# Kernel tuning notes

Hardware: AMD Instinct MI355X
Metric: run time of the kernel (lower is better)

The kernel has to match this reference:

```python
import jax, jax.numpy as jnp
import numpy as np
import math

D_MODEL = 512
N_HEAD = 8
D_K = D_MODEL // N_HEAD
BN_EPS = 1e-5


def setup_inputs() -> dict:
    key = jax.random.key(0)
    ks = jax.random.split(key, 24)
    B, L = 4, 2048
    s = 0.02
    inp = {
        'query': jax.random.normal(ks[0], (B, L, D_MODEL), jnp.float32),
        'key':   jax.random.normal(ks[1], (B, L, D_MODEL), jnp.float32),
        'value': jax.random.normal(ks[2], (B, L, D_MODEL), jnp.float32),
        # multi-scale conv (kernel sizes 3 and 5)
        'conv_w3': jax.random.normal(ks[3], (D_MODEL, D_MODEL, 3), jnp.float32) * s,
        'conv_b3': jnp.zeros((D_MODEL,), jnp.float32),
        'conv_w5': jax.random.normal(ks[4], (D_MODEL, D_MODEL, 5), jnp.float32) * s,
        'conv_b5': jnp.zeros((D_MODEL,), jnp.float32),
        # batchnorm over 2*d_model channels (inference mode, running stats)
        'bn_gamma': jnp.ones((2 * D_MODEL,), jnp.float32),
        'bn_beta':  jnp.zeros((2 * D_MODEL,), jnp.float32),
        'bn_mean':  jnp.zeros((2 * D_MODEL,), jnp.float32),
        'bn_var':   jnp.ones((2 * D_MODEL,), jnp.float32),
        # linear projections (torch layout: [out, in])
        'wq':  jax.random.normal(ks[5], (D_MODEL, D_MODEL), jnp.float32) * s,
        'bq':  jnp.zeros((D_MODEL,), jnp.float32),
        'wkl': jax.random.normal(ks[6], (D_MODEL, 2 * D_MODEL), jnp.float32) * s,
        'bkl': jnp.zeros((D_MODEL,), jnp.float32),
        'wkg': jax.random.normal(ks[7], (D_MODEL, D_MODEL), jnp.float32) * s,
        'bkg': jnp.zeros((D_MODEL,), jnp.float32),
        'wv':  jax.random.normal(ks[8], (D_MODEL, D_MODEL), jnp.float32) * s,
        'bv':  jnp.zeros((D_MODEL,), jnp.float32),
        'wo':  jax.random.normal(ks[9], (D_MODEL, D_MODEL), jnp.float32) * s,
        'bo':  jnp.zeros((D_MODEL,), jnp.float32),
    }
    return inp


def _conv1d_same(x_ncl, w_oik, b, pad):
    # x: [B, C_in, L], w: [C_out, C_in, K]
    y = jax.lax.conv_general_dilated(
        x_ncl, w_oik, window_strides=(1,), padding=[(pad, pad)],
        dimension_numbers=('NCH', 'OIH', 'NCH'))
    return y + b[None, :, None]


def _heads(x, B, L):
    # [B, L, D] -> [B, L, H, d_k]
    return x.reshape(B, L, N_HEAD, D_K)


def reference(query, key, value, conv_w3, conv_b3, conv_w5, conv_b5,
              bn_gamma, bn_beta, bn_mean, bn_var,
              wq, bq, wkl, bkl, wkg, bkg, wv, bv, wo, bo):
    B, L, _ = query.shape
    # local key path: multi-scale conv over sequence dim
    k_ncl = key.transpose(0, 2, 1)                      # [B, D, L]
    c3 = _conv1d_same(k_ncl, conv_w3, conv_b3, 1)       # [B, D, L]
    c5 = _conv1d_same(k_ncl, conv_w5, conv_b5, 2)       # [B, D, L]
    cat = jnp.concatenate([c3, c5], axis=1)             # [B, 2D, L]
    bn = (cat - bn_mean[None, :, None]) * (bn_gamma[None, :, None]
          * jax.lax.rsqrt(bn_var[None, :, None] + BN_EPS)) + bn_beta[None, :, None]
    key_local = bn.transpose(0, 2, 1)                   # [B, L, 2D]

    q  = _heads(query @ wq.T + bq, B, L)                # [B, L, H, dk]
    kl = _heads(key_local @ wkl.T + bkl, B, L)
    kg = _heads(key @ wkg.T + bkg, B, L)
    v  = _heads(value @ wv.T + bv, B, L)

    scale = 1.0 / math.sqrt(D_K)
    s_loc = jnp.einsum('bqhd,bkhd->bhqk', q, kl) * scale
    s_glo = jnp.einsum('bqhd,bkhd->bhqk', q, kg) * scale
    a_loc = jax.nn.softmax(s_loc, axis=-1)
    a_glo = jax.nn.softmax(s_glo, axis=-1)
    x = jnp.einsum('bhqk,bkhd->bqhd', a_loc, v) + jnp.einsum('bhqk,bkhd->bqhd', a_glo, v)
    x = x.reshape(B, L, N_HEAD * D_K)
    return x @ wo.T + bo
```

## Files before the change

### kernel.cpp

```cpp
#include <hip/hip_runtime.h>
#include <hip/hip_bf16.h>

#define D_MODEL 512
#define SEQ_L   2048
#define NBATCH  4
#define BLROWS  8192
#define BN_EPS_F 1e-5f
#define QK_SCALE 0.18033688011112042f

typedef __attribute__((ext_vector_type(8))) short bf16x8;
typedef __attribute__((ext_vector_type(4))) float f32x4;
typedef __attribute__((ext_vector_type(16))) float f32x16;
typedef __attribute__((ext_vector_type(2))) int i32x2;

__device__ __forceinline__ unsigned short f2bf(float f){
  union { float f; unsigned u; } x; x.f = f;
  return (unsigned short)((x.u + 0x7fffu + ((x.u >> 16) & 1u)) >> 16);
}
__device__ __forceinline__ unsigned pack2bf(float a, float b){
  return (unsigned)f2bf(a) | ((unsigned)f2bf(b) << 16);
}
__device__ __forceinline__ unsigned cvt_pk(float a, float b){
  unsigned r;
  asm("v_cvt_pk_bf16_f32 %0, %1, %2" : "=v"(r) : "v"(a), "v"(b));
  return r;
}
__device__ __forceinline__ float exp2fast(float x){
  float r;
  asm("v_exp_f32 %0, %1" : "=v"(r) : "v"(x));
  return r;
}
__device__ __forceinline__ float max3f(float a, float b, float c){
  float r;
  asm("v_max3_f32 %0, %1, %2, %3" : "=v"(r) : "v"(a), "v"(b), "v"(c));
  return r;
}
__device__ __forceinline__ f32x4 mfma16(bf16x8 a, bf16x8 b, f32x4 c){
  return __builtin_amdgcn_mfma_f32_16x16x32_bf16(a, b, c, 0, 0, 0);
}
__device__ __forceinline__ f32x16 mfma32(bf16x8 a, bf16x8 b, f32x16 c){
  return __builtin_amdgcn_mfma_f32_32x32x16_bf16(a, b, c, 0, 0, 0);
}
__device__ __forceinline__ bf16x8 ldb8(const unsigned short* p){
  return *reinterpret_cast<const bf16x8*>(p);
}
__device__ __forceinline__ void gld16(const void* g, void* l){
  __builtin_amdgcn_global_load_lds(
      (const __attribute__((address_space(1))) unsigned*)g,
      (__attribute__((address_space(3))) unsigned*)l, 16, 0, 0);
}

__global__ void k_cast3(const float* __restrict__ s0, const float* __restrict__ s1,
                        const float* __restrict__ s2, unsigned short* __restrict__ d0,
                        unsigned short* __restrict__ d1, unsigned short* __restrict__ d2,
                        int n){
  const int z = blockIdx.y;
  const float* s = (z == 0) ? s0 : (z == 1) ? s1 : s2;
  unsigned short* d = (z == 0) ? d0 : (z == 1) ? d1 : d2;
  int i = (blockIdx.x * blockDim.x + threadIdx.x) * 4;
  if (i >= n) return;
  float4 v = *reinterpret_cast<const float4*>(s + i);
  uint2 o;
  o.x = pack2bf(v.x, v.y);
  o.y = pack2bf(v.z, v.w);
  *reinterpret_cast<uint2*>(d + i) = o;
}

__global__ void k_cast4(const float* __restrict__ s0, const float* __restrict__ s1,
                        const float* __restrict__ s2, const float* __restrict__ s3,
                        unsigned short* __restrict__ d0, unsigned short* __restrict__ d1,
                        unsigned short* __restrict__ d2, unsigned short* __restrict__ d3,
                        int n, float sc0){
  const int z = blockIdx.y;
  const float* s = (z == 0) ? s0 : (z == 1) ? s1 : (z == 2) ? s2 : s3;
  unsigned short* d = (z == 0) ? d0 : (z == 1) ? d1 : (z == 2) ? d2 : d3;
  const float sc = (z == 0) ? sc0 : 1.f;
  int i = (blockIdx.x * blockDim.x + threadIdx.x) * 4;
  if (i >= n) return;
  float4 v = *reinterpret_cast<const float4*>(s + i);
  uint2 o;
  o.x = pack2bf(v.x * sc, v.y * sc);
  o.y = pack2bf(v.z * sc, v.w * sc);
  *reinterpret_cast<uint2*>(d + i) = o;
}

__global__ void k_acat(const float* __restrict__ wkl, const float* __restrict__ gamma,
                       const float* __restrict__ var, unsigned short* __restrict__ Acat){
  int idx = blockIdx.x * blockDim.x + threadIdx.x;
  int o = idx >> 10, ch = idx & 1023;
  int c = (ch < 512) ? (512 + ch) : (ch - 512);
  float a = gamma[c] * rsqrtf(var[c] + BN_EPS_F);
  Acat[idx] = f2bf(wkl[o * 1024 + c] * a);
}

__global__ void k_bcat(const float* __restrict__ w3, const float* __restrict__ w5,
                       unsigned short* __restrict__ Bcat){
  int idx = blockIdx.x * blockDim.x + threadIdx.x;
  int t = idx >> 19; int r = idx & 524287;
  int ci = r >> 10, ch = r & 1023;
  float v;
  if (ch < 512) v = w5[ch * 2560 + ci * 5 + t];
  else {
    int c3 = ch - 512;
    v = (t >= 1 && t <= 3) ? w3[c3 * 1536 + ci * 3 + (t - 1)] : 0.0f;
  }
  Bcat[idx] = f2bf(v);
}

__global__ void k_beff(const float* __restrict__ wkl, const float* __restrict__ gamma,
                       const float* __restrict__ beta, const float* __restrict__ mean,
                       const float* __restrict__ var, const float* __restrict__ cb3,
                       const float* __restrict__ cb5, const float* __restrict__ bkl,
                       float* __restrict__ beff){
  const int o = blockIdx.x * 4 + (threadIdx.x >> 6);
  const int lane = threadIdx.x & 63;
  float acc = 0.f;
  for (int c = lane; c < 1024; c += 64){
    float a = gamma[c] * rsqrtf(var[c] + BN_EPS_F);
    float cb = (c < 512) ? cb3[c] : cb5[c - 512];
    acc += wkl[o * 1024 + c] * (a * cb + beta[c] - a * mean[c]);
  }
#pragma unroll
  for (int off = 32; off; off >>= 1) acc += __shfl_down(acc, off);
  if (lane == 0) beff[o] = acc + bkl[o];
}

template<int MODE, int BN = 128>
__global__ __launch_bounds__(256, 2) void k_gemm(
    const unsigned short* __restrict__ A, const unsigned short* __restrict__ Bm,
    void* __restrict__ Cp, const float* __restrict__ bias,
    const float* __restrict__ bias1, const float* __restrict__ bias2, float bias_scale,
    int M, int N, int K, int lda, int ldb, int ldc,
    long sAz, long sBz, long sCz, const unsigned short* __restrict__ zeros)
{
  __shared__ unsigned short As[128 * 64];
  __shared__ unsigned short Bs[BN * 64];
  constexpr int NW2 = BN / 32;
  const int m0 = blockIdx.x * 128, n0 = blockIdx.y * BN;
  const unsigned short* Az = A + (long)blockIdx.z * sAz;
  const unsigned short* Bz = Bm + (long)blockIdx.z * sBz;
  const float* bz = bias; float bs = bias_scale;
  if (MODE == 3){
    if (blockIdx.z == 1){ bz = bias1; bs = 1.f; }
    else if (blockIdx.z == 2){ bz = bias2; bs = 1.f; }
  }
  const int tid = threadIdx.x, wid = tid >> 6, lane = tid & 63;
  const int l15 = lane & 15, hq = lane >> 4;
  const int wr = wid >> 1, wc = wid & 1;
  f32x4 acc[4][NW2];
#pragma unroll
  for (int m = 0; m < 4; ++m)
#pragma unroll
    for (int n = 0; n < NW2; ++n) acc[m][n] = f32x4{0.f, 0.f, 0.f, 0.f};
  const int nkt = K >> 6;
  const int wv4 = wid * 512;
  const int srow = tid >> 3;
  const int scol = (tid & 7) * 8;
  for (int kt = 0; kt < nkt; ++kt){
    __syncthreads();
    if (MODE == 2){
      const int t = kt >> 3; const int ci0 = (kt & 7) << 6;
#pragma unroll
      for (int i = 0; i < 4; ++i){
        int row = srow + i * 32;
        int gr = m0 + row;
        int sl = (gr & (SEQ_L - 1)) + t - 2;
        const unsigned short* sp = ((unsigned)sl < (unsigned)SEQ_L)
            ? (Az + (long)(gr + t - 2) * lda + ci0 + scol) : (zeros + scol);
        gld16(sp, As + i * 2048 + wv4);
      }
#pragma unroll
      for (int i = 0; i < BN / 32; ++i){
        int row = srow + i * 32;
        gld16(Bz + (long)t * 262144 + (long)(n0 + row) * ldb + ci0 + scol,
              Bs + i * 2048 + wv4);
      }
    } else {
      const int k0 = kt << 6;
#pragma unroll
      for (int i = 0; i < 4; ++i){
        int row = srow + i * 32;
        gld16(Az + (long)(m0 + row) * lda + k0 + scol, As + i * 2048 + wv4);
      }
#pragma unroll
      for (int i = 0; i < BN / 32; ++i){
        int row = srow + i * 32;
        gld16(Bz + (long)(n0 + row) * ldb + k0 + scol, Bs + i * 2048 + wv4);
      }
    }
    __syncthreads();
#pragma unroll
    for (int ks = 0; ks < 2; ++ks){
      const int kb = ks * 32 + 8 * hq;
      bf16x8 af[4], bfr[NW2];
#pragma unroll
      for (int m = 0; m < 4; ++m) af[m] = ldb8(As + (wr * 64 + m * 16 + l15) * 64 + kb);
#pragma unroll
      for (int n = 0; n < NW2; ++n)
        bfr[n] = ldb8(Bs + (wc * (BN / 2) + n * 16 + l15) * 64 + kb);
#pragma unroll
      for (int m = 0; m < 4; ++m)
#pragma unroll
        for (int n = 0; n < NW2; ++n) acc[m][n] = mfma16(af[m], bfr[n], acc[m][n]);
    }
  }
  const int crow0 = m0 + wr * 64, ccol0 = n0 + wc * (BN / 2);
#pragma unroll
  for (int n = 0; n < NW2; ++n){
    int col = ccol0 + n * 16 + l15;
    float bv = bz ? bz[col] * bs : 0.f;
#pragma unroll
    for (int m = 0; m < 4; ++m){
      int rowb = crow0 + m * 16 + 4 * hq;
#pragma unroll
      for (int r = 0; r < 4; ++r){
        float v = acc[m][n][r] + bv;
        long off = (long)(rowb + r) * ldc + col + (long)blockIdx.z * sCz;
        if (MODE == 1) ((float*)Cp)[off] = v;
        else ((unsigned short*)Cp)[off] = f2bf(v);
      }
    }
  }
}

__global__ __launch_bounds__(256) void k_transpose(const unsigned short* __restrict__ V,
                                                   unsigned short* __restrict__ Vt){
  __shared__ unsigned short t_lds[64][72];
  const int l0 = blockIdx.x * 64, d0 = blockIdx.y * 64, b = blockIdx.z;
  const int tid = threadIdx.x;
  const int rr = tid >> 3, cc = (tid & 7) * 8;
#pragma unroll
  for (int p = 0; p < 2; ++p){
    int r = rr + p * 32;
    bf16x8 v = ldb8(V + ((long)(b * SEQ_L + l0 + r)) * D_MODEL + d0 + cc);
#pragma unroll
    for (int j = 0; j < 8; ++j) t_lds[r][cc + j] = (unsigned short)v[j];
  }
  __syncthreads();
#pragma unroll
  for (int p = 0; p < 2; ++p){
    int dr = rr + p * 32;
    bf16x8 o;
#pragma unroll
    for (int j = 0; j < 8; ++j) o[j] = (short)t_lds[cc + j][dr];
    *reinterpret_cast<bf16x8*>(Vt + ((long)(b * D_MODEL + d0 + dr)) * SEQ_L + l0 + cc) = o;
  }
}

__global__ __launch_bounds__(256, 2) void k_attn(
    const unsigned short* __restrict__ Q, const unsigned short* __restrict__ KLp,
    const unsigned short* __restrict__ KGp, const unsigned short* __restrict__ Vt,
    unsigned short* __restrict__ X)
{
  __shared__ unsigned short KLb[2][64 * 64];
  __shared__ unsigned short KGb[2][64 * 64];
  __shared__ unsigned short Vb [2][64 * 64];

  const int lin = blockIdx.x + (blockIdx.y << 4);
  const int sw  = ((lin & 7) << 6) + (lin >> 3);
  const int qi = sw & 15, bh = sw >> 4;
  const int b = bh >> 3, hb = (bh & 7) << 6;
  const int tid = threadIdx.x, wid = tid >> 6, lane = tid & 63;
  const int l31 = lane & 31, hi = lane >> 5;
  const int s7 = l31 & 7;
  const int q0 = qi * 128 + wid * 32;
  const long rb = (long)b * SEQ_L;

  const long qrow = (rb + q0 + l31) * D_MODEL + hb + hi * 8;
  bf16x8 qf[4];
#pragma unroll
  for (int ch = 0; ch < 4; ++ch) qf[ch] = ldb8(Q + qrow + ch * 16);

  f32x16 o_l[2], o_g[2];
#pragma unroll
  for (int dt = 0; dt < 2; ++dt){ o_l[dt] = 0.f; o_g[dt] = 0.f; }
  float m_l = -1e30f, s_l = 0.f, m_g = -1e30f, s_g = 0.f;

  auto stage = [&](const unsigned short* gbase, long rowstride, unsigned short* lb){
#pragma unroll
    for (int i = 0; i < 2; ++i){
      const int idx0 = (i * 4 + wid) * 64;
      const int idx = idx0 + lane;
      const int row = idx >> 3, cl = idx & 7;
      const int cg = cl ^ (row & 7);
      gld16(gbase + (long)row * rowstride + cg * 8, lb + idx0 * 8);
    }
  };

  auto qk = [&](const unsigned short* Kb_, f32x16& sa, f32x16& sb){
    __builtin_amdgcn_s_setprio(1);
#pragma unroll
    for (int ch = 0; ch < 4; ++ch){
      bf16x8 k0 = ldb8(Kb_ + l31 * 64 + (((hi + 2 * ch) ^ s7) * 8));
      bf16x8 k1 = ldb8(Kb_ + (l31 + 32) * 64 + (((hi + 2 * ch) ^ s7) * 8));
      sa = mfma32(k0, qf[ch], sa);
      sb = mfma32(k1, qf[ch], sb);
    }
    __builtin_amdgcn_s_setprio(0);
  };

  auto softmax_pv = [&](f32x16& sa, f32x16& sb, float& mrun, float& srun,
                        f32x16 (&o)[2], bf16x8 (&vf)[2][4]){
    float u[8];
#pragma unroll
    for (int r = 0; r < 8; ++r)
      u[r] = max3f(sa[r], sa[r + 8], fmaxf(sb[r], sb[r + 8]));
    float pm = max3f(max3f(u[0], u[1], u[2]), max3f(u[3], u[4], u[5]),
                     fmaxf(u[6], u[7]));
    i32x2 pr = __builtin_amdgcn_permlane32_swap(__float_as_int(pm), __float_as_int(pm), false, false);
    pm = max3f(pm, __int_as_float(pr[0]), __int_as_float(pr[1]));
    if (__any(pm > mrun + 11.0f)){
      float mn = fmaxf(mrun, pm);
      float rs = exp2fast(mrun - mn);
      srun *= rs; mrun = mn;
#pragma unroll
      for (int r = 0; r < 16; ++r){ o[0][r] *= rs; o[1][r] *= rs; }
    }
#pragma unroll
    for (int r = 0; r < 16; ++r) sa[r] = exp2fast(sa[r] - mrun);
#pragma unroll
    for (int r = 0; r < 16; ++r) sb[r] = exp2fast(sb[r] - mrun);
    float w[8];
#pragma unroll
    for (int r = 0; r < 8; ++r) w[r] = (sa[r] + sa[r + 8]) + (sb[r] + sb[r + 8]);
    float sum = ((w[0] + w[1]) + (w[2] + w[3])) + ((w[4] + w[5]) + (w[6] + w[7]));
    i32x2 sr = __builtin_amdgcn_permlane32_swap(__float_as_int(sum), __float_as_int(sum), false, false);
    srun += __int_as_float(sr[0]) + __int_as_float(sr[1]);
    unsigned uu[2][4][2];
#pragma unroll
    for (int r4 = 0; r4 < 4; ++r4){
      uu[0][r4][0] = cvt_pk(sa[r4 * 4 + 0], sa[r4 * 4 + 1]);
      uu[0][r4][1] = cvt_pk(sa[r4 * 4 + 2], sa[r4 * 4 + 3]);
      uu[1][r4][0] = cvt_pk(sb[r4 * 4 + 0], sb[r4 * 4 + 1]);
      uu[1][r4][1] = cvt_pk(sb[r4 * 4 + 2], sb[r4 * 4 + 3]);
    }
    __builtin_amdgcn_s_setprio(1);
#pragma unroll
    for (int kc = 0; kc < 4; ++kc){
      const int t = kc >> 1, kk = kc & 1;
      i32x2 rA = __builtin_amdgcn_permlane32_swap((int)uu[t][2 * kk][0], (int)uu[t][2 * kk + 1][0], false, false);
      i32x2 rB = __builtin_amdgcn_permlane32_swap((int)uu[t][2 * kk][1], (int)uu[t][2 * kk + 1][1], false, false);
      union { bf16x8 v; int w_[4]; } pb;
      pb.w_[0] = rA[0]; pb.w_[1] = rB[0]; pb.w_[2] = rA[1]; pb.w_[3] = rB[1];
      o[0] = mfma32(vf[0][kc], pb.v, o[0]);
      o[1] = mfma32(vf[1][kc], pb.v, o[1]);
    }
    __builtin_amdgcn_s_setprio(0);
  };

  const unsigned short* klg = KLp + rb * D_MODEL + hb;
  const unsigned short* kgg = KGp + rb * D_MODEL + hb;
  const unsigned short* vtg = Vt + ((long)b * D_MODEL + hb) * SEQ_L;

  stage(klg, D_MODEL, KLb[0]);
  stage(kgg, D_MODEL, KGb[0]);
  stage(vtg, SEQ_L,  Vb[0]);
  asm volatile("s_waitcnt vmcnt(0)" ::: "memory");
  __syncthreads();

  int cur = 0;
#pragma unroll 1
  for (int t = 0; t < SEQ_L / 64; ++t){
    const int nxt = cur ^ 1;
    if (t < SEQ_L / 64 - 1){
      const long kvn = (long)(t + 1) * 64;
      stage(klg + kvn * D_MODEL, D_MODEL, KLb[nxt]);
      stage(kgg + kvn * D_MODEL, D_MODEL, KGb[nxt]);
      stage(vtg + kvn,           SEQ_L,   Vb[nxt]);
    }
    bf16x8 vf[2][4];
#pragma unroll
    for (int dt = 0; dt < 2; ++dt)
#pragma unroll
      for (int kc = 0; kc < 4; ++kc)
        vf[dt][kc] = ldb8(Vb[cur] + (l31 + dt * 32) * 64 + (((kc * 2 + hi) ^ s7) * 8));
    f32x16 sa = 0.f, sb = 0.f;
    qk(KLb[cur], sa, sb);
    softmax_pv(sa, sb, m_l, s_l, o_l, vf);
    f32x16 ga = 0.f, gb = 0.f;
    qk(KGb[cur], ga, gb);
    softmax_pv(ga, gb, m_g, s_g, o_g, vf);
    asm volatile("s_waitcnt vmcnt(0)" ::: "memory");
    __syncthreads();
    cur = nxt;
  }

  const float il = 1.f / s_l, ig = 1.f / s_g;
  const long xrow = (rb + q0 + l31) * D_MODEL + hb + hi * 4;
#pragma unroll
  for (int dt = 0; dt < 2; ++dt)
#pragma unroll
    for (int r4 = 0; r4 < 4; ++r4){
      float v0 = o_l[dt][r4 * 4 + 0] * il + o_g[dt][r4 * 4 + 0] * ig;
      float v1 = o_l[dt][r4 * 4 + 1] * il + o_g[dt][r4 * 4 + 1] * ig;
      float v2 = o_l[dt][r4 * 4 + 2] * il + o_g[dt][r4 * 4 + 2] * ig;
      float v3 = o_l[dt][r4 * 4 + 3] * il + o_g[dt][r4 * 4 + 3] * ig;
      uint2 pk2; pk2.x = cvt_pk(v0, v1); pk2.y = cvt_pk(v2, v3);
      *reinterpret_cast<uint2*>(X + xrow + dt * 32 + r4 * 8) = pk2;
    }
}

extern "C" void kernel_launch(void* const* d_in, const int* in_sizes, int n_in,
                              void* d_out, int out_size, void* d_ws, size_t ws_size,
                              hipStream_t stream)
{
  const float* query = (const float*)d_in[0];
  const float* key   = (const float*)d_in[1];
  const float* value = (const float*)d_in[2];
  const float* w3    = (const float*)d_in[3];
  const float* cb3   = (const float*)d_in[4];
  const float* w5    = (const float*)d_in[5];
  const float* cb5   = (const float*)d_in[6];
  const float* gamma = (const float*)d_in[7];
  const float* beta  = (const float*)d_in[8];
  const float* mean  = (const float*)d_in[9];
  const float* var   = (const float*)d_in[10];
  const float* wq    = (const float*)d_in[11];
  const float* bq    = (const float*)d_in[12];
  const float* wkl   = (const float*)d_in[13];
  const float* bkl   = (const float*)d_in[14];
  const float* wkg   = (const float*)d_in[15];
  const float* bkg   = (const float*)d_in[16];
  const float* wv    = (const float*)d_in[17];
  const float* bv    = (const float*)d_in[18];
  const float* wo    = (const float*)d_in[19];
  const float* bo    = (const float*)d_in[20];

  char* ws = (char*)d_ws;
  const size_t MB = 1024 * 1024;
  unsigned short* qb   = (unsigned short*)(ws + 0 * MB);
  unsigned short* kb   = (unsigned short*)(ws + 8 * MB);
  unsigned short* vb   = (unsigned short*)(ws + 16 * MB);
  unsigned short* Qm   = (unsigned short*)(ws + 24 * MB);
  unsigned short* KGm  = (unsigned short*)(ws + 32 * MB);
  unsigned short* Vm   = (unsigned short*)(ws + 40 * MB);
  unsigned short* KLm  = (unsigned short*)(ws + 48 * MB);
  unsigned short* Vt   = qb;
  unsigned short* Xm   = vb;
  unsigned short* Bcat = Qm;
  unsigned short* Acat = KGm;
  unsigned short* Weff = (unsigned short*)(ws + 56 * MB);
  unsigned short* wqb  = (unsigned short*)(ws + 56 * MB + 2621440);
  unsigned short* wkgb = wqb + 262144;
  unsigned short* wvb  = wqb + 524288;
  unsigned short* wob  = wqb + 786432;
  float*          beff = (float*)(ws + 61 * MB);
  unsigned short* zeros= (unsigned short*)(ws + 61 * MB + 4096);

  hipMemsetAsync(zeros, 0, 256, stream);

  const int NQKV = BLROWS * D_MODEL;
  const int NW   = D_MODEL * D_MODEL;
  dim3 tb(256);
  k_cast3<<<dim3(NQKV / 1024, 3), tb, 0, stream>>>(query, key, value, qb, kb, vb, NQKV);
  k_cast4<<<dim3(NW / 1024, 4), tb, 0, stream>>>(wq, wkg, wv, wo, wqb, wkgb, wvb, wob,
                                                 NW, QK_SCALE);
  k_acat<<<(512 * 1024) / 256, tb, 0, stream>>>(wkl, gamma, var, Acat);
  k_bcat<<<(5 * 512 * 1024) / 256, tb, 0, stream>>>(w3, w5, Bcat);
  k_beff<<<128, tb, 0, stream>>>(wkl, gamma, beta, mean, var, cb3, cb5, bkl, beff);

  k_gemm<0><<<dim3(4, 4, 5), tb, 0, stream>>>(Acat, Bcat, Weff,
      nullptr, nullptr, nullptr, 0.f,
      512, 512, 1024, 1024, 1024, 512, 0L, 524288L, 262144L, nullptr);

  k_gemm<3><<<dim3(64, 4, 3), tb, 0, stream>>>(qb, wqb, Qm,
      bq, bkg, bv, QK_SCALE,
      BLROWS, D_MODEL, D_MODEL, D_MODEL, D_MODEL, D_MODEL,
      4194304L, 262144L, 4194304L, nullptr);

  k_gemm<2, 64><<<dim3(64, 8), tb, 0, stream>>>(kb, Weff, KLm,
      beff, nullptr, nullptr, 1.f,
      BLROWS, D_MODEL, 2560, D_MODEL, D_MODEL, D_MODEL, 0L, 0L, 0L, zeros);

  k_transpose<<<dim3(32, 8, 4), tb, 0, stream>>>(Vm, Vt);
  k_attn<<<dim3(16, 32), tb, 0, stream>>>(Qm, KLm, KGm, Vt, Xm);

  k_gemm<1><<<dim3(64, 4), tb, 0, stream>>>(Xm, wob, d_out,
      bo, nullptr, nullptr, 1.f,
      BLROWS, D_MODEL, D_MODEL, D_MODEL, D_MODEL, D_MODEL, 0L, 0L, 0L, nullptr);
}
```

Measured before the change: 245.8 us.

## Split local and global attention paths across separate wave groups in attention kernel

The attention block grows from 256 to 512 threads. Waves 0-3 now handle the local-key softmax path and waves 4-7 handle the global-key path, where before each wave ran both paths one after the other. Staging work is spread over all eight waves, and V fragments are read from LDS inside the PV loop instead of being preloaded. At the end, the global path writes its normalized output to shared memory and the local-path waves add it in and store. This doubles the number of waves working on the same tile and lowers per-wave register pressure, at the cost of an extra LDS reduction and barrier and fewer resident blocks per CU.

```diff
diff --git a/kernel.cpp b/kernel.cpp
--- a/kernel.cpp
+++ b/kernel.cpp
@@ -247,23 +247,22 @@
   }
 }
 
-__global__ __launch_bounds__(256, 2) void k_attn(
+__global__ __launch_bounds__(512, 2) void k_attn(
     const unsigned short* __restrict__ Q, const unsigned short* __restrict__ KLp,
     const unsigned short* __restrict__ KGp, const unsigned short* __restrict__ Vt,
     unsigned short* __restrict__ X)
 {
-  __shared__ unsigned short KLb[2][64 * 64];
-  __shared__ unsigned short KGb[2][64 * 64];
-  __shared__ unsigned short Vb [2][64 * 64];
+  __shared__ unsigned short smem[6][4096];
 
   const int lin = blockIdx.x + (blockIdx.y << 4);
   const int sw  = ((lin & 7) << 6) + (lin >> 3);
   const int qi = sw & 15, bh = sw >> 4;
   const int b = bh >> 3, hb = (bh & 7) << 6;
   const int tid = threadIdx.x, wid = tid >> 6, lane = tid & 63;
+  const int path = wid >> 2, wg = wid & 3;
   const int l31 = lane & 31, hi = lane >> 5;
   const int s7 = l31 & 7;
-  const int q0 = qi * 128 + wid * 32;
+  const int q0 = qi * 128 + wg * 32;
   const long rb = (long)b * SEQ_L;
 
   const long qrow = (rb + q0 + l31) * D_MODEL + hb + hi * 8;
@@ -271,23 +270,41 @@
 #pragma unroll
   for (int ch = 0; ch < 4; ++ch) qf[ch] = ldb8(Q + qrow + ch * 16);
 
-  f32x16 o_l[2], o_g[2];
-#pragma unroll
-  for (int dt = 0; dt < 2; ++dt){ o_l[dt] = 0.f; o_g[dt] = 0.f; }
-  float m_l = -1e30f, s_l = 0.f, m_g = -1e30f, s_g = 0.f;
+  f32x16 o[2];
+  o[0] = 0.f; o[1] = 0.f;
+  float mrun = -1e30f, srun = 0.f;
 
   auto stage = [&](const unsigned short* gbase, long rowstride, unsigned short* lb){
-#pragma unroll
-    for (int i = 0; i < 2; ++i){
-      const int idx0 = (i * 4 + wid) * 64;
-      const int idx = idx0 + lane;
-      const int row = idx >> 3, cl = idx & 7;
-      const int cg = cl ^ (row & 7);
-      gld16(gbase + (long)row * rowstride + cg * 8, lb + idx0 * 8);
-    }
+    const int idx0 = wid * 64;
+    const int idx = idx0 + lane;
+    const int row = idx >> 3, cl = idx & 7;
+    const int cg = cl ^ (row & 7);
+    gld16(gbase + (long)row * rowstride + cg * 8, lb + idx0 * 8);
   };
 
-  auto qk = [&](const unsigned short* Kb_, f32x16& sa, f32x16& sb){
+  const unsigned short* klg = KLp + rb * D_MODEL + hb;
+  const unsigned short* kgg = KGp + rb * D_MODEL + hb;
+  const unsigned short* vtg = Vt + ((long)b * D_MODEL + hb) * SEQ_L;
+
+  stage(klg, D_MODEL, smem[0]);
+  stage(kgg, D_MODEL, smem[2]);
+  stage(vtg, SEQ_L,  smem[4]);
+  asm volatile("s_waitcnt vmcnt(0)" ::: "memory");
+  __syncthreads();
+
+  int cur = 0;
+#pragma unroll 1
+  for (int t = 0; t < SEQ_L / 64; ++t){
+    const int nxt = cur ^ 1;
+    if (t < SEQ_L / 64 - 1){
+      const long kvn = (long)(t + 1) * 64;
+      stage(klg + kvn * D_MODEL, D_MODEL, smem[nxt]);
+      stage(kgg + kvn * D_MODEL, D_MODEL, smem[2 + nxt]);
+      stage(vtg + kvn,           SEQ_L,   smem[4 + nxt]);
+    }
+    const unsigned short* Kb_ = path ? smem[2 + cur] : smem[cur];
+    const unsigned short* Vb_ = smem[4 + cur];
+    f32x16 sa = 0.f, sb = 0.f;
     __builtin_amdgcn_s_setprio(1);
 #pragma unroll
     for (int ch = 0; ch < 4; ++ch){
@@ -297,10 +314,6 @@
       sb = mfma32(k1, qf[ch], sb);
     }
     __builtin_amdgcn_s_setprio(0);
-  };
-
-  auto softmax_pv = [&](f32x16& sa, f32x16& sb, float& mrun, float& srun,
-                        f32x16 (&o)[2], bf16x8 (&vf)[2][4]){
     float u[8];
 #pragma unroll
     for (int r = 0; r < 8; ++r)
@@ -337,67 +350,47 @@
     __builtin_amdgcn_s_setprio(1);
 #pragma unroll
     for (int kc = 0; kc < 4; ++kc){
-      const int t = kc >> 1, kk = kc & 1;
-      i32x2 rA = __builtin_amdgcn_permlane32_swap((int)uu[t][2 * kk][0], (int)uu[t][2 * kk + 1][0], false, false);
-      i32x2 rB = __builtin_amdgcn_permlane32_swap((int)uu[t][2 * kk][1], (int)uu[t][2 * kk + 1][1], false, false);
+      const int tt = kc >> 1, kk = kc & 1;
+      i32x2 rA = __builtin_amdgcn_permlane32_swap((int)uu[tt][2 * kk][0], (int)uu[tt][2 * kk + 1][0], false, false);
+      i32x2 rB = __builtin_amdgcn_permlane32_swap((int)uu[tt][2 * kk][1], (int)uu[tt][2 * kk + 1][1], false, false);
       union { bf16x8 v; int w_[4]; } pb;
       pb.w_[0] = rA[0]; pb.w_[1] = rB[0]; pb.w_[2] = rA[1]; pb.w_[3] = rB[1];
-      o[0] = mfma32(vf[0][kc], pb.v, o[0]);
-      o[1] = mfma32(vf[1][kc], pb.v, o[1]);
+      bf16x8 v0 = ldb8(Vb_ + l31 * 64 + (((kc * 2 + hi) ^ s7) * 8));
+      bf16x8 v1 = ldb8(Vb_ + (l31 + 32) * 64 + (((kc * 2 + hi) ^ s7) * 8));
+      o[0] = mfma32(v0, pb.v, o[0]);
+      o[1] = mfma32(v1, pb.v, o[1]);
     }
     __builtin_amdgcn_s_setprio(0);
-  };
-
-  const unsigned short* klg = KLp + rb * D_MODEL + hb;
-  const unsigned short* kgg = KGp + rb * D_MODEL + hb;
-  const unsigned short* vtg = Vt + ((long)b * D_MODEL + hb) * SEQ_L;
-
-  stage(klg, D_MODEL, KLb[0]);
-  stage(kgg, D_MODEL, KGb[0]);
-  stage(vtg, SEQ_L,  Vb[0]);
-  asm volatile("s_waitcnt vmcnt(0)" ::: "memory");
-  __syncthreads();
-
-  int cur = 0;
-#pragma unroll 1
-  for (int t = 0; t < SEQ_L / 64; ++t){
-    const int nxt = cur ^ 1;
-    if (t < SEQ_L / 64 - 1){
-      const long kvn = (long)(t + 1) * 64;
-      stage(klg + kvn * D_MODEL, D_MODEL, KLb[nxt]);
-      stage(kgg + kvn * D_MODEL, D_MODEL, KGb[nxt]);
-      stage(vtg + kvn,           SEQ_L,   Vb[nxt]);
-    }
-    bf16x8 vf[2][4];
-#pragma unroll
-    for (int dt = 0; dt < 2; ++dt)
-#pragma unroll
-      for (int kc = 0; kc < 4; ++kc)
-        vf[dt][kc] = ldb8(Vb[cur] + (l31 + dt * 32) * 64 + (((kc * 2 + hi) ^ s7) * 8));
-    f32x16 sa = 0.f, sb = 0.f;
-    qk(KLb[cur], sa, sb);
-    softmax_pv(sa, sb, m_l, s_l, o_l, vf);
-    f32x16 ga = 0.f, gb = 0.f;
-    qk(KGb[cur], ga, gb);
-    softmax_pv(ga, gb, m_g, s_g, o_g, vf);
     asm volatile("s_waitcnt vmcnt(0)" ::: "memory");
     __syncthreads();
     cur = nxt;
   }
 
-  const float il = 1.f / s_l, ig = 1.f / s_g;
-  const long xrow = (rb + q0 + l31) * D_MODEL + hb + hi * 4;
-#pragma unroll
-  for (int dt = 0; dt < 2; ++dt)
-#pragma unroll
-    for (int r4 = 0; r4 < 4; ++r4){
-      float v0 = o_l[dt][r4 * 4 + 0] * il + o_g[dt][r4 * 4 + 0] * ig;
-      float v1 = o_l[dt][r4 * 4 + 1] * il + o_g[dt][r4 * 4 + 1] * ig;
-      float v2 = o_l[dt][r4 * 4 + 2] * il + o_g[dt][r4 * 4 + 2] * ig;
-      float v3 = o_l[dt][r4 * 4 + 3] * il + o_g[dt][r4 * 4 + 3] * ig;
-      uint2 pk2; pk2.x = cvt_pk(v0, v1); pk2.y = cvt_pk(v2, v3);
-      *reinterpret_cast<uint2*>(X + xrow + dt * 32 + r4 * 8) = pk2;
-    }
+  float* shF = (float*)smem;
+  const int mb = (wg * 64 + lane) * 32;
+  const float inv = 1.f / srun;
+  if (path){
+#pragma unroll
+    for (int r = 0; r < 16; ++r){
+      shF[mb + r]      = o[0][r] * inv;
+      shF[mb + 16 + r] = o[1][r] * inv;
+    }
+  }
+  __syncthreads();
+  if (!path){
+    const long xrow = (rb + q0 + l31) * D_MODEL + hb + hi * 4;
+#pragma unroll
+    for (int dt = 0; dt < 2; ++dt)
+#pragma unroll
+      for (int r4 = 0; r4 < 4; ++r4){
+        float v0 = o[dt][r4 * 4 + 0] * inv + shF[mb + dt * 16 + r4 * 4 + 0];
+        float v1 = o[dt][r4 * 4 + 1] * inv + shF[mb + dt * 16 + r4 * 4 + 1];
+        float v2 = o[dt][r4 * 4 + 2] * inv + shF[mb + dt * 16 + r4 * 4 + 2];
+        float v3 = o[dt][r4 * 4 + 3] * inv + shF[mb + dt * 16 + r4 * 4 + 3];
+        uint2 pk2; pk2.x = cvt_pk(v0, v1); pk2.y = cvt_pk(v2, v3);
+        *reinterpret_cast<uint2*>(X + xrow + dt * 32 + r4 * 8) = pk2;
+      }
+  }
 }
 
 extern "C" void kernel_launch(void* const* d_in, const int* in_sizes, int n_in,
@@ -473,7 +466,7 @@
       BLROWS, D_MODEL, 2560, D_MODEL, D_MODEL, D_MODEL, 0L, 0L, 0L, zeros);
 
   k_transpose<<<dim3(32, 8, 4), tb, 0, stream>>>(Vm, Vt);
-  k_attn<<<dim3(16, 32), tb, 0, stream>>>(Qm, KLm, KGm, Vt, Xm);
+  k_attn<<<dim3(16, 32), dim3(512), 0, stream>>>(Qm, KLm, KGm, Vt, Xm);
 
   k_gemm<1><<<dim3(64, 4), tb, 0, stream>>>(Xm, wob, d_out,
       bo, nullptr, nullptr, 1.f,
```

After: 238.3 us. 3.0% less time.
